# Kernel optimization log

Hardware: AMD Instinct MI355X
Metric: run time of the kernel (lower is better)

The kernel has to match this reference:

```python
import jax, jax.numpy as jnp
import numpy as np

B, P, E, NH = 256, 512, 12, 4  # batch, points, attention_dim, nheads


def _mha(xq, xk, xv, in_w, in_b, out_w, out_b, nheads=NH):
    # torch.nn.MultiheadAttention (batch_first): packed in_proj [3E,E], out_proj [E,E]
    Ed = xq.shape[-1]
    D = Ed // nheads
    wq, wk, wv = jnp.split(in_w, 3, axis=0)
    bq, bk, bv = jnp.split(in_b, 3)
    q = (xq @ wq.T + bq).reshape(xq.shape[0], xq.shape[1], nheads, D)
    k = (xk @ wk.T + bk).reshape(xk.shape[0], xk.shape[1], nheads, D)
    v = (xv @ wv.T + bv).reshape(xv.shape[0], xv.shape[1], nheads, D)
    scale = 1.0 / jnp.sqrt(jnp.asarray(D, dtype=q.dtype))
    att = jax.nn.softmax(jnp.einsum('bqhd,bkhd->bhqk', q, k) * scale, axis=-1)
    o = jnp.einsum('bhqk,bkhd->bqhd', att, v).reshape(xq.shape[0], xq.shape[1], Ed)
    return o @ out_w.T + out_b


def _kabsch(A, Bp):
    # n_dim_rigid_transform_Kabsch_3D_torch; note: reflect() in the source always
    # builds SS = identity (both branches identical), so R = U @ Vt exactly.
    cA = A.mean(axis=1, keepdims=True)  # [B,1,3]
    cB = Bp.mean(axis=1, keepdims=True)
    Am = A - cA
    Bm = Bp - cB
    Hm = jnp.einsum('bpi,bpj->bij', Bm, Am)  # [B,3,3]
    U, S, Vt = jnp.linalg.svd(Hm)
    R = U @ Vt
    t = cA - cB @ R
    return R, t


def setup_inputs() -> dict:
    key = jax.random.key(0)
    ks = jax.random.split(key, 22)
    w = lambda k, s: jax.random.normal(k, s, dtype=jnp.float32) * 0.1
    return {
        'x_orig': jax.random.normal(ks[0], (B, P, 3), dtype=jnp.float32),
        'y_orig': jax.random.normal(ks[1], (B, P, 3), dtype=jnp.float32),
        'lin_in_w': w(ks[2], (E, 3)), 'lin_in_b': w(ks[3], (E,)),
        'lin_in2_w': w(ks[4], (E, 3)), 'lin_in2_b': w(ks[5], (E,)),
        'attn_in_w': w(ks[6], (3 * E, E)), 'attn_in_b': w(ks[7], (3 * E,)),
        'attn_out_w': w(ks[8], (E, E)), 'attn_out_b': w(ks[9], (E,)),
        'attn2_in_w': w(ks[10], (3 * E, E)), 'attn2_in_b': w(ks[11], (3 * E,)),
        'attn2_out_w': w(ks[12], (E, E)), 'attn2_out_b': w(ks[13], (E,)),
        'cross_in_w': w(ks[14], (3 * E, E)), 'cross_in_b': w(ks[15], (3 * E,)),
        'cross_out_w': w(ks[16], (E, E)), 'cross_out_b': w(ks[17], (E,)),
        'lin_out_w': w(ks[18], (3, E)), 'lin_out_b': w(ks[19], (3,)),
    }


def reference(x_orig, y_orig, lin_in_w, lin_in_b, lin_in2_w, lin_in2_b,
              attn_in_w, attn_in_b, attn_out_w, attn_out_b,
              attn2_in_w, attn2_in_b, attn2_out_w, attn2_out_b,
              cross_in_w, cross_in_b, cross_out_w, cross_out_b,
              lin_out_w, lin_out_b):
    x = x_orig - x_orig.mean(axis=1, keepdims=True)
    y_translate = y_orig.mean(axis=1, keepdims=True)
    y = y_orig - y_translate
    xi = x @ lin_in_w.T + lin_in_b
    yi = y @ lin_in2_w.T + lin_in2_b
    xi = _mha(xi, xi, xi, attn_in_w, attn_in_b, attn_out_w, attn_out_b)
    yi = _mha(yi, yi, yi, attn2_in_w, attn2_in_b, attn2_out_w, attn2_out_b)
    cross = _mha(xi, yi, yi, cross_in_w, cross_in_b, cross_out_w, cross_out_b)
    coords = cross @ lin_out_w.T + lin_out_b  # [B,P,3]
    R, t = _kabsch(coords + x, x)
    return x @ R + t + y_translate
```

## Files before the change

### kernel.cpp

```cpp
#include <hip/hip_runtime.h>
#include <math.h>

#define NB   256
#define PTS  512
#define EMB  12
#define NHD  4

typedef short short8v __attribute__((ext_vector_type(8)));
typedef float floatx4 __attribute__((ext_vector_type(4)));

union U16 { uint4 u; short8v s; };

__device__ __forceinline__ unsigned bf16rne(float x) {
  union { float f; unsigned u; } v; v.f = x;
  return (v.u + 0x7FFFu + ((v.u >> 16) & 1u)) >> 16;
}

template<int N>
__device__ __forceinline__ void block_reduce(float* v, float* sred, int t) {
  const int lane = t & 63;
  const int wv   = t >> 6;
  #pragma unroll
  for (int i = 0; i < N; ++i) {
    float s = v[i];
    #pragma unroll
    for (int off = 32; off > 0; off >>= 1) s += __shfl_down(s, off, 64);
    if (lane == 0) sred[wv * N + i] = s;
  }
  __syncthreads();
  #pragma unroll
  for (int i = 0; i < N; ++i) {
    float s = 0.f;
    #pragma unroll
    for (int w = 0; w < 8; ++w) s += sred[w * N + i];
    v[i] = s;
  }
  __syncthreads();
}

__device__ __forceinline__ void mha_mfma(
    const float* qin, const float* kvin,
    const float* __restrict__ w_in, const float* __restrict__ b_in,
    const float* __restrict__ w_out, const float* __restrict__ b_out,
    float* outv,
    uint4* skA, uint4* sqQ, unsigned short* svB, float* sO, int t)
{
  __syncthreads();

  {
    const float qs = 0.5773502691896258f * 1.4426950408889634f;
    float kk[EMB], vv[EMB], qq[EMB];
    #pragma unroll
    for (int e = 0; e < EMB; ++e) {
      float q_ = b_in[e], k_ = b_in[EMB + e], v_ = b_in[2 * EMB + e];
      #pragma unroll
      for (int f = 0; f < EMB; ++f) {
        q_ = fmaf(qin[f],  w_in[e * EMB + f],             q_);
        k_ = fmaf(kvin[f], w_in[(EMB + e) * EMB + f],     k_);
        v_ = fmaf(kvin[f], w_in[(2 * EMB + e) * EMB + f], v_);
      }
      qq[e] = q_ * qs; kk[e] = k_; vv[e] = v_;
    }
    const int kt = t >> 4, kap = t & 15;
    const int grp = t >> 5, g = t & 31;
    const int odd = g >> 4, sub = g & 15;
    const int q4 = sub >> 2, jj = (sub & 3) + 4 * odd;
    #pragma unroll
    for (int h = 0; h < NHD; ++h) {
      skA[(kt * NHD + h) * 16 + kap] =
          make_uint4(bf16rne(kk[h*3]) | (bf16rne(kk[h*3+1]) << 16), bf16rne(kk[h*3+2]), 0u, 0u);
      sqQ[(kt * NHD + h) * 16 + kap] =
          make_uint4(bf16rne(qq[h*3]) | (bf16rne(qq[h*3+1]) << 16), bf16rne(qq[h*3+2]), 0u, 0u);
      #pragma unroll
      for (int n = 0; n < 4; ++n) {
        float vval = (n < 3) ? vv[h*3+n] : 1.0f;
        svB[(((grp * NHD + h) * 4 + q4) * 4 + n) * 8 + jj] = (unsigned short)bf16rne(vval);
      }
    }
  }
  __syncthreads();

  const int lane = t & 63, wv = t >> 6;
  const int lq = lane >> 4, ln = lane & 15;

  short8v qf[4][NHD];
  #pragma unroll
  for (int i = 0; i < 4; ++i)
    #pragma unroll
    for (int h = 0; h < NHD; ++h) {
      U16 u; u.u = sqQ[((wv * 4 + i) * NHD + h) * 16 + ln];
      if (lq != 0) u.u = make_uint4(0u, 0u, 0u, 0u);
      qf[i][h] = u.s;
    }

  floatx4 oacc[4][NHD];
  #pragma unroll
  for (int i = 0; i < 4; ++i)
    #pragma unroll
    for (int h = 0; h < NHD; ++h) {
      floatx4 z = {0.f, 0.f, 0.f, 0.f};
      oacc[i][h] = z;
    }

  const uint4* svB4 = (const uint4*)svB;
  for (int kg = 0; kg < 16; ++kg) {
    #pragma unroll
    for (int h = 0; h < NHD; ++h) {
      U16 ke, ko, vf;
      ke.u = skA[((2 * kg + 0) * NHD + h) * 16 + ln];
      ko.u = skA[((2 * kg + 1) * NHD + h) * 16 + ln];
      vf.u = svB4[((kg * NHD + h) * 4 + lq) * 4 + (ln & 3)];
      #pragma unroll
      for (int i = 0; i < 4; ++i) {
        floatx4 zc = {0.f, 0.f, 0.f, 0.f};
        floatx4 se = __builtin_amdgcn_mfma_f32_16x16x32_bf16(ke.s, qf[i][h], zc, 0, 0, 0);
        floatx4 so = __builtin_amdgcn_mfma_f32_16x16x32_bf16(ko.s, qf[i][h], zc, 0, 0, 0);
        unsigned p0 = __float_as_uint(__builtin_amdgcn_exp2f(se[0]));
        unsigned p1 = __float_as_uint(__builtin_amdgcn_exp2f(se[1]));
        unsigned p2 = __float_as_uint(__builtin_amdgcn_exp2f(se[2]));
        unsigned p3 = __float_as_uint(__builtin_amdgcn_exp2f(se[3]));
        unsigned p4 = __float_as_uint(__builtin_amdgcn_exp2f(so[0]));
        unsigned p5 = __float_as_uint(__builtin_amdgcn_exp2f(so[1]));
        unsigned p6 = __float_as_uint(__builtin_amdgcn_exp2f(so[2]));
        unsigned p7 = __float_as_uint(__builtin_amdgcn_exp2f(so[3]));
        U16 pf;
        pf.u.x = __builtin_amdgcn_perm(p1, p0, 0x07060302u);
        pf.u.y = __builtin_amdgcn_perm(p3, p2, 0x07060302u);
        pf.u.z = __builtin_amdgcn_perm(p5, p4, 0x07060302u);
        pf.u.w = __builtin_amdgcn_perm(p7, p6, 0x07060302u);
        oacc[i][h] = __builtin_amdgcn_mfma_f32_16x16x32_bf16(pf.s, vf.s, oacc[i][h], 0, 0, 0);
      }
    }
  }

  if (ln < 4) {
    #pragma unroll
    for (int i = 0; i < 4; ++i)
      #pragma unroll
      for (int h = 0; h < NHD; ++h)
        #pragma unroll
        for (int r = 0; r < 4; ++r)
          sO[((wv * 4 + i) * 16 + lq * 4 + r) * 16 + h * 4 + ln] = oacc[i][h][r];
  }
  __syncthreads();

  {
    const float4* sr = (const float4*)(sO + t * 16);
    float o[EMB];
    #pragma unroll
    for (int h = 0; h < NHD; ++h) {
      float4 Oh = sr[h];
      float inv = 1.0f / fmaxf(Oh.w, 1e-20f);
      o[h*3+0] = Oh.x * inv; o[h*3+1] = Oh.y * inv; o[h*3+2] = Oh.z * inv;
    }
    #pragma unroll
    for (int e = 0; e < EMB; ++e) {
      float s = b_out[e];
      #pragma unroll
      for (int f = 0; f < EMB; ++f) s = fmaf(o[f], w_out[e * EMB + f], s);
      outv[e] = s;
    }
  }
}

__global__ __launch_bounds__(512, 2)
void pcr_kernel(const float* __restrict__ x_orig, const float* __restrict__ y_orig,
                const float* __restrict__ lin_in_w,  const float* __restrict__ lin_in_b,
                const float* __restrict__ lin_in2_w, const float* __restrict__ lin_in2_b,
                const float* __restrict__ attn_in_w,  const float* __restrict__ attn_in_b,
                const float* __restrict__ attn_out_w, const float* __restrict__ attn_out_b,
                const float* __restrict__ attn2_in_w,  const float* __restrict__ attn2_in_b,
                const float* __restrict__ attn2_out_w, const float* __restrict__ attn2_out_b,
                const float* __restrict__ cross_in_w,  const float* __restrict__ cross_in_b,
                const float* __restrict__ cross_out_w, const float* __restrict__ cross_out_b,
                const float* __restrict__ lin_out_w, const float* __restrict__ lin_out_b,
                float* __restrict__ out)
{
  __shared__ __align__(16) uint4 skA[32 * NHD * 16];
  __shared__ __align__(16) uint4 sqQ[32 * NHD * 16];
  __shared__ __align__(16) unsigned short svB[16 * NHD * 4 * 4 * 8];
  __shared__ __align__(16) float sO[PTS * 16];
  __shared__ float sred[8 * 12];

  const int b = blockIdx.x;
  const int t = threadIdx.x;
  const int base = (b * PTS + t) * 3;

  float x3[3], y3[3], ymean[3];
  {
    float r6[6];
    #pragma unroll
    for (int i = 0; i < 3; ++i) r6[i]     = x_orig[base + i];
    #pragma unroll
    for (int i = 0; i < 3; ++i) r6[3 + i] = y_orig[base + i];
    float xl[3] = {r6[0], r6[1], r6[2]};
    float yl[3] = {r6[3], r6[4], r6[5]};
    block_reduce<6>(r6, sred, t);
    #pragma unroll
    for (int i = 0; i < 3; ++i) {
      x3[i]    = xl[i] - r6[i] * (1.f / PTS);
      ymean[i] = r6[3 + i] * (1.f / PTS);
      y3[i]    = yl[i] - ymean[i];
    }
  }

  float xi[EMB], yi[EMB];
  #pragma unroll
  for (int e = 0; e < EMB; ++e) {
    float sx = lin_in_b[e], sy = lin_in2_b[e];
    #pragma unroll
    for (int i = 0; i < 3; ++i) {
      sx = fmaf(x3[i], lin_in_w[e * 3 + i], sx);
      sy = fmaf(y3[i], lin_in2_w[e * 3 + i], sy);
    }
    xi[e] = sx; yi[e] = sy;
  }

  float tmp[EMB];
  mha_mfma(xi, xi, attn_in_w,  attn_in_b,  attn_out_w,  attn_out_b,  tmp, skA, sqQ, svB, sO, t);
  #pragma unroll
  for (int e = 0; e < EMB; ++e) xi[e] = tmp[e];
  mha_mfma(yi, yi, attn2_in_w, attn2_in_b, attn2_out_w, attn2_out_b, tmp, skA, sqQ, svB, sO, t);
  #pragma unroll
  for (int e = 0; e < EMB; ++e) yi[e] = tmp[e];
  mha_mfma(xi, yi, cross_in_w, cross_in_b, cross_out_w, cross_out_b, tmp, skA, sqQ, svB, sO, t);

  float bp[3];
  #pragma unroll
  for (int d = 0; d < 3; ++d) {
    float c = lin_out_b[d];
    #pragma unroll
    for (int e = 0; e < EMB; ++e) c = fmaf(tmp[e], lin_out_w[d * EMB + e], c);
    bp[d] = c + x3[d];
  }

  float r12[12];
  #pragma unroll
  for (int i = 0; i < 3; ++i)
    #pragma unroll
    for (int j = 0; j < 3; ++j) r12[i * 3 + j] = x3[i] * bp[j];
  #pragma unroll
  for (int j = 0; j < 3; ++j) r12[9 + j] = bp[j];
  block_reduce<12>(r12, sred, t);

  float cA[3];
  #pragma unroll
  for (int j = 0; j < 3; ++j) cA[j] = r12[9 + j] * (1.f / PTS);

  float a00 = r12[0], a01 = r12[1], a02 = r12[2];
  float a10 = r12[3], a11 = r12[4], a12_ = r12[5];
  float a20 = r12[6], a21 = r12[7], a22 = r12[8];

  float c0 = fabsf(a00) + fabsf(a10) + fabsf(a20);
  float c1 = fabsf(a01) + fabsf(a11) + fabsf(a21);
  float c2 = fabsf(a02) + fabsf(a12_) + fabsf(a22);
  float r0 = fabsf(a00) + fabsf(a01) + fabsf(a02);
  float r1 = fabsf(a10) + fabsf(a11) + fabsf(a12_);
  float r2 = fabsf(a20) + fabsf(a21) + fabsf(a22);
  float fsc = rsqrtf(fmaxf(c0, fmaxf(c1, c2)) * fmaxf(r0, fmaxf(r1, r2)) + 1e-30f);
  a00 *= fsc; a01 *= fsc; a02 *= fsc;
  a10 *= fsc; a11 *= fsc; a12_ *= fsc;
  a20 *= fsc; a21 *= fsc; a22 *= fsc;

  #pragma unroll 1
  for (int it = 0; it < 12; ++it) {
    float C00 = a11*a22 - a12_*a21;
    float C01 = a12_*a20 - a10*a22;
    float C02 = a10*a21 - a11*a20;
    float C10 = a02*a21 - a01*a22;
    float C11 = a00*a22 - a02*a20;
    float C12 = a01*a20 - a00*a21;
    float C20 = a01*a12_ - a02*a11;
    float C21 = a02*a10 - a00*a12_;
    float C22 = a00*a11 - a01*a10;
    float det = a00*C00 + a01*C01 + a02*C02;
    float g  = 1.0f / cbrtf(fabsf(det) + 1e-30f);
    float dg = det * g;
    dg = copysignf(fmaxf(fabsf(dg), 1e-25f), dg);
    float id = 0.5f / dg;
    float gh = 0.5f * g;
    a00 = gh*a00 + C00*id; a01 = gh*a01 + C01*id; a02 = gh*a02 + C02*id;
    a10 = gh*a10 + C10*id; a11 = gh*a11 + C11*id; a12_ = gh*a12_ + C12*id;
    a20 = gh*a20 + C20*id; a21 = gh*a21 + C21*id; a22 = gh*a22 + C22*id;
  }

  float o0 = fmaf(x3[0], a00, fmaf(x3[1], a10, fmaf(x3[2], a20, cA[0] + ymean[0])));
  float o1 = fmaf(x3[0], a01, fmaf(x3[1], a11, fmaf(x3[2], a21, cA[1] + ymean[1])));
  float o2 = fmaf(x3[0], a02, fmaf(x3[1], a12_, fmaf(x3[2], a22, cA[2] + ymean[2])));
  out[base + 0] = o0;
  out[base + 1] = o1;
  out[base + 2] = o2;
}

extern "C" void kernel_launch(void* const* d_in, const int* in_sizes, int n_in,
                              void* d_out, int out_size, void* d_ws, size_t ws_size,
                              hipStream_t stream) {
  const float* p[20];
  for (int i = 0; i < 20; ++i) p[i] = (const float*)d_in[i];
  pcr_kernel<<<dim3(NB), dim3(512), 0, stream>>>(
      p[0], p[1], p[2], p[3], p[4], p[5], p[6], p[7], p[8], p[9],
      p[10], p[11], p[12], p[13], p[14], p[15], p[16], p[17], p[18], p[19],
      (float*)d_out);
}
```

Baseline: 213.0 us.

## Use 1024-thread blocks splitting Q and K/V projection and attention rows

Doubles the block to 1024 threads. The upper half computes Q projections while the lower half computes K/V, and each wave now handles 2 query tiles instead of 4, halving per-thread MFMA work and register pressure. Even and odd key tiles are packed into one uint4 load with a denser K layout. The point-wise work is duplicated across the two halves and guarded for the output. The cost is more threads per block, larger reductions, and duplicated projection/epilogue arithmetic.

```diff
diff --git a/kernel.cpp b/kernel.cpp
--- a/kernel.cpp
+++ b/kernel.cpp
@@ -16,7 +16,7 @@
   return (v.u + 0x7FFFu + ((v.u >> 16) & 1u)) >> 16;
 }
 
-template<int N>
+template<int N, int NW>
 __device__ __forceinline__ void block_reduce(float* v, float* sred, int t) {
   const int lane = t & 63;
   const int wv   = t >> 6;
@@ -32,7 +32,7 @@
   for (int i = 0; i < N; ++i) {
     float s = 0.f;
     #pragma unroll
-    for (int w = 0; w < 8; ++w) s += sred[w * N + i];
+    for (int w = 0; w < NW; ++w) s += sred[w * N + i];
     v[i] = s;
   }
   __syncthreads();
@@ -47,55 +47,67 @@
 {
   __syncthreads();
 
-  {
-    const float qs = 0.5773502691896258f * 1.4426950408889634f;
-    float kk[EMB], vv[EMB], qq[EMB];
+  const int p = t & 511;
+  if (t < 512) {
+    float kk[EMB], vv[EMB];
     #pragma unroll
     for (int e = 0; e < EMB; ++e) {
-      float q_ = b_in[e], k_ = b_in[EMB + e], v_ = b_in[2 * EMB + e];
+      float k_ = b_in[EMB + e], v_ = b_in[2 * EMB + e];
       #pragma unroll
       for (int f = 0; f < EMB; ++f) {
-        q_ = fmaf(qin[f],  w_in[e * EMB + f],             q_);
         k_ = fmaf(kvin[f], w_in[(EMB + e) * EMB + f],     k_);
         v_ = fmaf(kvin[f], w_in[(2 * EMB + e) * EMB + f], v_);
       }
-      qq[e] = q_ * qs; kk[e] = k_; vv[e] = v_;
-    }
-    const int kt = t >> 4, kap = t & 15;
-    const int grp = t >> 5, g = t & 31;
-    const int odd = g >> 4, sub = g & 15;
+      kk[e] = k_; vv[e] = v_;
+    }
+    const int kg = p >> 5, oddt = (p >> 4) & 1, kap = p & 15;
+    uint2* skA2 = (uint2*)skA;
+    const int g = p & 31, odd = g >> 4, sub = g & 15;
     const int q4 = sub >> 2, jj = (sub & 3) + 4 * odd;
     #pragma unroll
     for (int h = 0; h < NHD; ++h) {
-      skA[(kt * NHD + h) * 16 + kap] =
-          make_uint4(bf16rne(kk[h*3]) | (bf16rne(kk[h*3+1]) << 16), bf16rne(kk[h*3+2]), 0u, 0u);
+      skA2[((kg * NHD + h) * 16 + kap) * 2 + oddt] =
+          make_uint2(bf16rne(kk[h*3]) | (bf16rne(kk[h*3+1]) << 16), bf16rne(kk[h*3+2]));
+      #pragma unroll
+      for (int n = 0; n < 4; ++n) {
+        float vval = (n < 3) ? vv[h*3+n] : 1.0f;
+        svB[(((kg * NHD + h) * 4 + q4) * 4 + n) * 8 + jj] = (unsigned short)bf16rne(vval);
+      }
+    }
+  } else {
+    const float qs = 0.5773502691896258f * 1.4426950408889634f;
+    float qq[EMB];
+    #pragma unroll
+    for (int e = 0; e < EMB; ++e) {
+      float q_ = b_in[e];
+      #pragma unroll
+      for (int f = 0; f < EMB; ++f) q_ = fmaf(qin[f], w_in[e * EMB + f], q_);
+      qq[e] = q_ * qs;
+    }
+    const int kt = p >> 4, kap = p & 15;
+    #pragma unroll
+    for (int h = 0; h < NHD; ++h)
       sqQ[(kt * NHD + h) * 16 + kap] =
           make_uint4(bf16rne(qq[h*3]) | (bf16rne(qq[h*3+1]) << 16), bf16rne(qq[h*3+2]), 0u, 0u);
-      #pragma unroll
-      for (int n = 0; n < 4; ++n) {
-        float vval = (n < 3) ? vv[h*3+n] : 1.0f;
-        svB[(((grp * NHD + h) * 4 + q4) * 4 + n) * 8 + jj] = (unsigned short)bf16rne(vval);
-      }
-    }
   }
   __syncthreads();
 
   const int lane = t & 63, wv = t >> 6;
   const int lq = lane >> 4, ln = lane & 15;
 
-  short8v qf[4][NHD];
-  #pragma unroll
-  for (int i = 0; i < 4; ++i)
-    #pragma unroll
-    for (int h = 0; h < NHD; ++h) {
-      U16 u; u.u = sqQ[((wv * 4 + i) * NHD + h) * 16 + ln];
+  short8v qf[2][NHD];
+  #pragma unroll
+  for (int i = 0; i < 2; ++i)
+    #pragma unroll
+    for (int h = 0; h < NHD; ++h) {
+      U16 u; u.u = sqQ[((wv * 2 + i) * NHD + h) * 16 + ln];
       if (lq != 0) u.u = make_uint4(0u, 0u, 0u, 0u);
       qf[i][h] = u.s;
     }
 
-  floatx4 oacc[4][NHD];
-  #pragma unroll
-  for (int i = 0; i < 4; ++i)
+  floatx4 oacc[2][NHD];
+  #pragma unroll
+  for (int i = 0; i < 2; ++i)
     #pragma unroll
     for (int h = 0; h < NHD; ++h) {
       floatx4 z = {0.f, 0.f, 0.f, 0.f};
@@ -106,15 +118,15 @@
   for (int kg = 0; kg < 16; ++kg) {
     #pragma unroll
     for (int h = 0; h < NHD; ++h) {
-      U16 ke, ko, vf;
-      ke.u = skA[((2 * kg + 0) * NHD + h) * 16 + ln];
-      ko.u = skA[((2 * kg + 1) * NHD + h) * 16 + ln];
-      vf.u = svB4[((kg * NHD + h) * 4 + lq) * 4 + (ln & 3)];
-      #pragma unroll
-      for (int i = 0; i < 4; ++i) {
+      uint4 kp = skA[(kg * NHD + h) * 16 + ln];
+      U16 vf; vf.u = svB4[((kg * NHD + h) * 4 + lq) * 4 + (ln & 3)];
+      U16 fe; fe.u = make_uint4(kp.x, kp.y, 0u, 0u);
+      U16 fo; fo.u = make_uint4(kp.z, kp.w, 0u, 0u);
+      #pragma unroll
+      for (int i = 0; i < 2; ++i) {
         floatx4 zc = {0.f, 0.f, 0.f, 0.f};
-        floatx4 se = __builtin_amdgcn_mfma_f32_16x16x32_bf16(ke.s, qf[i][h], zc, 0, 0, 0);
-        floatx4 so = __builtin_amdgcn_mfma_f32_16x16x32_bf16(ko.s, qf[i][h], zc, 0, 0, 0);
+        floatx4 se = __builtin_amdgcn_mfma_f32_16x16x32_bf16(fe.s, qf[i][h], zc, 0, 0, 0);
+        floatx4 so = __builtin_amdgcn_mfma_f32_16x16x32_bf16(fo.s, qf[i][h], zc, 0, 0, 0);
         unsigned p0 = __float_as_uint(__builtin_amdgcn_exp2f(se[0]));
         unsigned p1 = __float_as_uint(__builtin_amdgcn_exp2f(se[1]));
         unsigned p2 = __float_as_uint(__builtin_amdgcn_exp2f(se[2]));
@@ -135,17 +147,17 @@
 
   if (ln < 4) {
     #pragma unroll
-    for (int i = 0; i < 4; ++i)
+    for (int i = 0; i < 2; ++i)
       #pragma unroll
       for (int h = 0; h < NHD; ++h)
         #pragma unroll
         for (int r = 0; r < 4; ++r)
-          sO[((wv * 4 + i) * 16 + lq * 4 + r) * 16 + h * 4 + ln] = oacc[i][h][r];
+          sO[((wv * 2 + i) * 16 + lq * 4 + r) * 16 + h * 4 + ln] = oacc[i][h][r];
   }
   __syncthreads();
 
   {
-    const float4* sr = (const float4*)(sO + t * 16);
+    const float4* sr = (const float4*)(sO + p * 16);
     float o[EMB];
     #pragma unroll
     for (int h = 0; h < NHD; ++h) {
@@ -163,7 +175,7 @@
   }
 }
 
-__global__ __launch_bounds__(512, 2)
+__global__ __launch_bounds__(1024, 4)
 void pcr_kernel(const float* __restrict__ x_orig, const float* __restrict__ y_orig,
                 const float* __restrict__ lin_in_w,  const float* __restrict__ lin_in_b,
                 const float* __restrict__ lin_in2_w, const float* __restrict__ lin_in2_b,
@@ -176,26 +188,29 @@
                 const float* __restrict__ lin_out_w, const float* __restrict__ lin_out_b,
                 float* __restrict__ out)
 {
-  __shared__ __align__(16) uint4 skA[32 * NHD * 16];
+  __shared__ __align__(16) uint4 skA[16 * NHD * 16];
   __shared__ __align__(16) uint4 sqQ[32 * NHD * 16];
   __shared__ __align__(16) unsigned short svB[16 * NHD * 4 * 4 * 8];
   __shared__ __align__(16) float sO[PTS * 16];
-  __shared__ float sred[8 * 12];
+  __shared__ float sred[16 * 12];
 
   const int b = blockIdx.x;
   const int t = threadIdx.x;
-  const int base = (b * PTS + t) * 3;
-
-  float x3[3], y3[3], ymean[3];
+  const int p = t & 511;
+  const bool own = (t < 512);
+  const int base = (b * PTS + p) * 3;
+
+  float x3[3], y3[3], ymean[3], xl[3], yl[3];
   {
+    #pragma unroll
+    for (int i = 0; i < 3; ++i) { xl[i] = x_orig[base + i]; yl[i] = y_orig[base + i]; }
     float r6[6];
     #pragma unroll
-    for (int i = 0; i < 3; ++i) r6[i]     = x_orig[base + i];
-    #pragma unroll
-    for (int i = 0; i < 3; ++i) r6[3 + i] = y_orig[base + i];
-    float xl[3] = {r6[0], r6[1], r6[2]};
-    float yl[3] = {r6[3], r6[4], r6[5]};
-    block_reduce<6>(r6, sred, t);
+    for (int i = 0; i < 3; ++i) {
+      r6[i]     = own ? xl[i] : 0.f;
+      r6[3 + i] = own ? yl[i] : 0.f;
+    }
+    block_reduce<6, 16>(r6, sred, t);
     #pragma unroll
     for (int i = 0; i < 3; ++i) {
       x3[i]    = xl[i] - r6[i] * (1.f / PTS);
@@ -238,58 +253,60 @@
   #pragma unroll
   for (int i = 0; i < 3; ++i)
     #pragma unroll
-    for (int j = 0; j < 3; ++j) r12[i * 3 + j] = x3[i] * bp[j];
-  #pragma unroll
-  for (int j = 0; j < 3; ++j) r12[9 + j] = bp[j];
-  block_reduce<12>(r12, sred, t);
-
-  float cA[3];
-  #pragma unroll
-  for (int j = 0; j < 3; ++j) cA[j] = r12[9 + j] * (1.f / PTS);
-
-  float a00 = r12[0], a01 = r12[1], a02 = r12[2];
-  float a10 = r12[3], a11 = r12[4], a12_ = r12[5];
-  float a20 = r12[6], a21 = r12[7], a22 = r12[8];
-
-  float c0 = fabsf(a00) + fabsf(a10) + fabsf(a20);
-  float c1 = fabsf(a01) + fabsf(a11) + fabsf(a21);
-  float c2 = fabsf(a02) + fabsf(a12_) + fabsf(a22);
-  float r0 = fabsf(a00) + fabsf(a01) + fabsf(a02);
-  float r1 = fabsf(a10) + fabsf(a11) + fabsf(a12_);
-  float r2 = fabsf(a20) + fabsf(a21) + fabsf(a22);
-  float fsc = rsqrtf(fmaxf(c0, fmaxf(c1, c2)) * fmaxf(r0, fmaxf(r1, r2)) + 1e-30f);
-  a00 *= fsc; a01 *= fsc; a02 *= fsc;
-  a10 *= fsc; a11 *= fsc; a12_ *= fsc;
-  a20 *= fsc; a21 *= fsc; a22 *= fsc;
-
-  #pragma unroll 1
-  for (int it = 0; it < 12; ++it) {
-    float C00 = a11*a22 - a12_*a21;
-    float C01 = a12_*a20 - a10*a22;
-    float C02 = a10*a21 - a11*a20;
-    float C10 = a02*a21 - a01*a22;
-    float C11 = a00*a22 - a02*a20;
-    float C12 = a01*a20 - a00*a21;
-    float C20 = a01*a12_ - a02*a11;
-    float C21 = a02*a10 - a00*a12_;
-    float C22 = a00*a11 - a01*a10;
-    float det = a00*C00 + a01*C01 + a02*C02;
-    float g  = 1.0f / cbrtf(fabsf(det) + 1e-30f);
-    float dg = det * g;
-    dg = copysignf(fmaxf(fabsf(dg), 1e-25f), dg);
-    float id = 0.5f / dg;
-    float gh = 0.5f * g;
-    a00 = gh*a00 + C00*id; a01 = gh*a01 + C01*id; a02 = gh*a02 + C02*id;
-    a10 = gh*a10 + C10*id; a11 = gh*a11 + C11*id; a12_ = gh*a12_ + C12*id;
-    a20 = gh*a20 + C20*id; a21 = gh*a21 + C21*id; a22 = gh*a22 + C22*id;
-  }
-
-  float o0 = fmaf(x3[0], a00, fmaf(x3[1], a10, fmaf(x3[2], a20, cA[0] + ymean[0])));
-  float o1 = fmaf(x3[0], a01, fmaf(x3[1], a11, fmaf(x3[2], a21, cA[1] + ymean[1])));
-  float o2 = fmaf(x3[0], a02, fmaf(x3[1], a12_, fmaf(x3[2], a22, cA[2] + ymean[2])));
-  out[base + 0] = o0;
-  out[base + 1] = o1;
-  out[base + 2] = o2;
+    for (int j = 0; j < 3; ++j) r12[i * 3 + j] = own ? x3[i] * bp[j] : 0.f;
+  #pragma unroll
+  for (int j = 0; j < 3; ++j) r12[9 + j] = own ? bp[j] : 0.f;
+  block_reduce<12, 16>(r12, sred, t);
+
+  if (own) {
+    float cA[3];
+    #pragma unroll
+    for (int j = 0; j < 3; ++j) cA[j] = r12[9 + j] * (1.f / PTS);
+
+    float a00 = r12[0], a01 = r12[1], a02 = r12[2];
+    float a10 = r12[3], a11 = r12[4], a12_ = r12[5];
+    float a20 = r12[6], a21 = r12[7], a22 = r12[8];
+
+    float c0 = fabsf(a00) + fabsf(a10) + fabsf(a20);
+    float c1 = fabsf(a01) + fabsf(a11) + fabsf(a21);
+    float c2 = fabsf(a02) + fabsf(a12_) + fabsf(a22);
+    float r0 = fabsf(a00) + fabsf(a01) + fabsf(a02);
+    float r1 = fabsf(a10) + fabsf(a11) + fabsf(a12_);
+    float r2 = fabsf(a20) + fabsf(a21) + fabsf(a22);
+    float fsc = rsqrtf(fmaxf(c0, fmaxf(c1, c2)) * fmaxf(r0, fmaxf(r1, r2)) + 1e-30f);
+    a00 *= fsc; a01 *= fsc; a02 *= fsc;
+    a10 *= fsc; a11 *= fsc; a12_ *= fsc;
+    a20 *= fsc; a21 *= fsc; a22 *= fsc;
+
+    #pragma unroll 1
+    for (int it = 0; it < 12; ++it) {
+      float C00 = a11*a22 - a12_*a21;
+      float C01 = a12_*a20 - a10*a22;
+      float C02 = a10*a21 - a11*a20;
+      float C10 = a02*a21 - a01*a22;
+      float C11 = a00*a22 - a02*a20;
+      float C12 = a01*a20 - a00*a21;
+      float C20 = a01*a12_ - a02*a11;
+      float C21 = a02*a10 - a00*a12_;
+      float C22 = a00*a11 - a01*a10;
+      float det = a00*C00 + a01*C01 + a02*C02;
+      float g  = 1.0f / cbrtf(fabsf(det) + 1e-30f);
+      float dg = det * g;
+      dg = copysignf(fmaxf(fabsf(dg), 1e-25f), dg);
+      float id = 0.5f / dg;
+      float gh = 0.5f * g;
+      a00 = gh*a00 + C00*id; a01 = gh*a01 + C01*id; a02 = gh*a02 + C02*id;
+      a10 = gh*a10 + C10*id; a11 = gh*a11 + C11*id; a12_ = gh*a12_ + C12*id;
+      a20 = gh*a20 + C20*id; a21 = gh*a21 + C21*id; a22 = gh*a22 + C22*id;
+    }
+
+    float o0 = fmaf(x3[0], a00, fmaf(x3[1], a10, fmaf(x3[2], a20, cA[0] + ymean[0])));
+    float o1 = fmaf(x3[0], a01, fmaf(x3[1], a11, fmaf(x3[2], a21, cA[1] + ymean[1])));
+    float o2 = fmaf(x3[0], a02, fmaf(x3[1], a12_, fmaf(x3[2], a22, cA[2] + ymean[2])));
+    out[base + 0] = o0;
+    out[base + 1] = o1;
+    out[base + 2] = o2;
+  }
 }
 
 extern "C" void kernel_launch(void* const* d_in, const int* in_sizes, int n_in,
@@ -297,7 +314,7 @@
                               hipStream_t stream) {
   const float* p[20];
   for (int i = 0; i < 20; ++i) p[i] = (const float*)d_in[i];
-  pcr_kernel<<<dim3(NB), dim3(512), 0, stream>>>(
+  pcr_kernel<<<dim3(NB), dim3(1024), 0, stream>>>(
       p[0], p[1], p[2], p[3], p[4], p[5], p[6], p[7], p[8], p[9],
       p[10], p[11], p[12], p[13], p[14], p[15], p[16], p[17], p[18], p[19],
       (float*)d_out);
```

After: 240.2 us. 1.13x slower.
